# Performance work log

Hardware: AMD Instinct MI355X
Metric: run time of the kernel (lower is better)

Reference implementation:

```python
import jax, jax.numpy as jnp
import numpy as np

B=4; L=1024; NF=64; DM=256; DS=16; SCS=8; NL=4; DI=512; DTR=16; DC=4; NFM=6; NH=4; SCALES=(5,20,50)

def _ln(x,g,b):
    m=x.mean(-1,keepdims=True); v=((x-m)**2).mean(-1,keepdims=True)
    return (x-m)*jax.lax.rsqrt(v+1e-5)*g+b

def _scan(dA,dBu,C):
    # sequential selective scan: h_t = dA_t*h + dBu_t ; y_t = sum_n h_t * C_t
    def step(h,inp):
        a,bu,c=inp
        h=a*h+bu
        return h, jnp.einsum('bdn,bn->bd',h,c)
    h0=jnp.zeros(dA.shape[:1]+dA.shape[2:],dA.dtype)
    _,ys=jax.lax.scan(step,h0,(dA.swapaxes(0,1),dBu.swapaxes(0,1),C.swapaxes(0,1)))
    return ys.swapaxes(0,1)  # [B,L,DI]

def _mamba(x,g,b,inw,cw,cb,xpw,dtw,dtb,Alog,Dp,outw,ds):
    # MambaBlock: LN -> SelectiveSSM -> residual (dropout=identity in eval)
    xn=_ln(x,g,b)
    u,z=jnp.split(xn@inw.T,2,-1)
    k=cw.T[:,None,:]  # torch depthwise Conv1d weight [DI,1,DC] -> WIO [DC,1,DI]
    u=jax.lax.conv_general_dilated(u,k,(1,),[(cw.shape[1]-1,0)],dimension_numbers=('NWC','WIO','NWC'),feature_group_count=u.shape[-1])+cb
    u=jax.nn.silu(u)
    A=-jnp.exp(Alog)                     # [DI,ds]
    xd=u@xpw.T                           # [B,L,DTR+2*ds]
    dt=jax.nn.softplus(xd[...,:DTR]@dtw.T+dtb)   # [B,L,DI]
    Bm=xd[...,DTR:DTR+ds]; Cm=xd[...,DTR+ds:]
    dA=jnp.exp(dt[...,None]*A)                   # [B,L,DI,ds]
    dBu=dt[...,None]*Bm[:,:,None,:]*u[...,None]  # [B,L,DI,ds]
    y=_scan(dA,dBu,Cm)+u*Dp
    return x+(y*jax.nn.silu(z))@outw.T

def _mha(x,wqkv,bqkv,wout,bout):
    Bq,S,E=x.shape; hd=E//NH
    q,k,v=jnp.split(x@wqkv.T+bqkv,3,-1)
    sp=lambda t: t.reshape(Bq,S,NH,hd).transpose(0,2,1,3)
    att=jax.nn.softmax(jnp.einsum('bhqd,bhkd->bhqk',sp(q),sp(k))*(1.0/np.sqrt(hd)),-1)
    o=jnp.einsum('bhqk,bhkd->bhqd',att,sp(v)).transpose(0,2,1,3).reshape(Bq,S,E)
    return o@wout.T+bout

def _forward(x,in_w,in_b,in_ln_g,in_ln_b,mb_ln_g,mb_ln_b,mb_in_w,mb_conv_w,mb_conv_b,mb_xp_w,mb_dt_w,mb_dt_b,mb_Alog,mb_D,mb_out_w,sc_ln_g,sc_ln_b,sc_in_w,sc_conv_w,sc_conv_b,sc_xp_w,sc_dt_w,sc_dt_b,sc_Alog,sc_D,sc_out_w,fus_qkv_w,fus_qkv_b,fus_out_w,fus_out_b,ms_out_w,ms_out_b,sa_ln1_g,sa_ln1_b,sa_ln2_g,sa_ln2_b,sa_qkv_w,sa_qkv_b,sa_out_w,sa_out_b,sa_ff1_w,sa_ff1_b,sa_ff2_w,sa_ff2_b,ev1_w,ev1_b,ev2_w,ev2_b,ttf1_w,ttf1_b,ttf2_w,ttf2_b,emb_w,emb_b):
    gelu=lambda t: jax.nn.gelu(t,approximate=False)
    h=gelu(_ln(x@in_w.T+in_b,in_ln_g,in_ln_b))
    for i in range(NL):
        h=_mamba(h,mb_ln_g[i],mb_ln_b[i],mb_in_w[i],mb_conv_w[i],mb_conv_b[i],mb_xp_w[i],mb_dt_w[i],mb_dt_b[i],mb_Alog[i],mb_D[i],mb_out_w[i],DS)
    pooled=[]
    for i,s in enumerate(SCALES):
        p=_mamba(h[:,-s:,:],sc_ln_g[i],sc_ln_b[i],sc_in_w[i],sc_conv_w[i],sc_conv_b[i],sc_xp_w[i],sc_dt_w[i],sc_dt_b[i],sc_Alog[i],sc_D[i],sc_out_w[i],SCS)
        pooled.append(p.mean(1))  # AdaptiveAvgPool1d(1)
    stack=jnp.stack(pooled,1)  # [B,3,DM]
    fused=_mha(stack,fus_qkv_w,fus_qkv_b,fus_out_w,fus_out_b).reshape(x.shape[0],-1)@ms_out_w.T+ms_out_b
    s2=stack+_mha(_ln(stack,sa_ln1_g,sa_ln1_b),sa_qkv_w,sa_qkv_b,sa_out_w,sa_out_b)
    att=s2+(gelu(_ln(s2,sa_ln2_g,sa_ln2_b)@sa_ff1_w.T+sa_ff1_b)@sa_ff2_w.T+sa_ff2_b)
    final=fused+att.mean(1)
    ev=jax.nn.softplus(gelu(final@ev1_w.T+ev1_b)@ev2_w.T+ev2_b)
    alpha=ev+1.0
    Ssum=alpha.sum(-1,keepdims=True)
    probs=alpha/Ssum; unc=(NFM+1)/Ssum
    ttf=gelu(final@ttf1_w.T+ttf1_b)@ttf2_w.T+ttf2_b
    tm=jax.nn.softplus(ttf[:,:NFM]); ts=jnp.exp(0.5*ttf[:,NFM:])
    emb=final@emb_w.T+emb_b
    # concat of (probs, evidence, alpha, uncertainty, ttf_mean, ttf_std, embedding) -> [B,162]
    return jnp.concatenate([probs,ev,alpha,unc,tm,ts,emb],-1)

def setup_inputs():
    ks=iter(jax.random.split(jax.random.key(0),64))
    nk=lambda: next(ks)
    w=lambda *s: jax.random.normal(nk(),s,jnp.float32)*0.02
    z=lambda *s: jnp.zeros(s,jnp.float32)
    o=lambda *s: jnp.ones(s,jnp.float32)
    Al=lambda n,ds: jnp.broadcast_to(jnp.log(jnp.arange(1,ds+1,dtype=jnp.float32)),(n,DI,ds))
    return dict(x=jax.random.normal(nk(),(B,L,NF),jnp.float32),
        in_w=w(DM,NF), in_b=z(DM), in_ln_g=o(DM), in_ln_b=z(DM),
        mb_ln_g=o(NL,DM), mb_ln_b=z(NL,DM), mb_in_w=w(NL,2*DI,DM), mb_conv_w=w(NL,DI,DC), mb_conv_b=z(NL,DI),
        mb_xp_w=w(NL,DTR+2*DS,DI), mb_dt_w=w(NL,DI,DTR), mb_dt_b=z(NL,DI), mb_Alog=Al(NL,DS), mb_D=o(NL,DI), mb_out_w=w(NL,DM,DI),
        sc_ln_g=o(3,DM), sc_ln_b=z(3,DM), sc_in_w=w(3,2*DI,DM), sc_conv_w=w(3,DI,DC), sc_conv_b=z(3,DI),
        sc_xp_w=w(3,DTR+2*SCS,DI), sc_dt_w=w(3,DI,DTR), sc_dt_b=z(3,DI), sc_Alog=Al(3,SCS), sc_D=o(3,DI), sc_out_w=w(3,DM,DI),
        fus_qkv_w=w(3*DM,DM), fus_qkv_b=z(3*DM), fus_out_w=w(DM,DM), fus_out_b=z(DM), ms_out_w=w(DM,3*DM), ms_out_b=z(DM),
        sa_ln1_g=o(DM), sa_ln1_b=z(DM), sa_ln2_g=o(DM), sa_ln2_b=z(DM),
        sa_qkv_w=w(3*DM,DM), sa_qkv_b=z(3*DM), sa_out_w=w(DM,DM), sa_out_b=z(DM),
        sa_ff1_w=w(4*DM,DM), sa_ff1_b=z(4*DM), sa_ff2_w=w(DM,4*DM), sa_ff2_b=z(DM),
        ev1_w=w(DM,DM), ev1_b=z(DM), ev2_w=w(NFM+1,DM), ev2_b=z(NFM+1),
        ttf1_w=w(DM//2,DM), ttf1_b=z(DM//2), ttf2_w=w(2*NFM,DM//2), ttf2_b=z(2*NFM),
        emb_w=w(DM//2,DM), emb_b=z(DM//2))

def reference(x,in_w,in_b,in_ln_g,in_ln_b,mb_ln_g,mb_ln_b,mb_in_w,mb_conv_w,mb_conv_b,mb_xp_w,mb_dt_w,mb_dt_b,mb_Alog,mb_D,mb_out_w,sc_ln_g,sc_ln_b,sc_in_w,sc_conv_w,sc_conv_b,sc_xp_w,sc_dt_w,sc_dt_b,sc_Alog,sc_D,sc_out_w,fus_qkv_w,fus_qkv_b,fus_out_w,fus_out_b,ms_out_w,ms_out_b,sa_ln1_g,sa_ln1_b,sa_ln2_g,sa_ln2_b,sa_qkv_w,sa_qkv_b,sa_out_w,sa_out_b,sa_ff1_w,sa_ff1_b,sa_ff2_w,sa_ff2_b,ev1_w,ev1_b,ev2_w,ev2_b,ttf1_w,ttf1_b,ttf2_w,ttf2_b,emb_w,emb_b):
    return _forward(x,in_w,in_b,in_ln_g,in_ln_b,mb_ln_g,mb_ln_b,mb_in_w,mb_conv_w,mb_conv_b,mb_xp_w,mb_dt_w,mb_dt_b,mb_Alog,mb_D,mb_out_w,sc_ln_g,sc_ln_b,sc_in_w,sc_conv_w,sc_conv_b,sc_xp_w,sc_dt_w,sc_dt_b,sc_Alog,sc_D,sc_out_w,fus_qkv_w,fus_qkv_b,fus_out_w,fus_out_b,ms_out_w,ms_out_b,sa_ln1_g,sa_ln1_b,sa_ln2_g,sa_ln2_b,sa_qkv_w,sa_qkv_b,sa_out_w,sa_out_b,sa_ff1_w,sa_ff1_b,sa_ff2_w,sa_ff2_b,ev1_w,ev1_b,ev2_w,ev2_b,ttf1_w,ttf1_b,ttf2_w,ttf2_b,emb_w,emb_b)
```

## Files before the change

### kernel.cpp

```cpp
#include <hip/hip_runtime.h>
#include <math.h>


typedef short short8v __attribute__((ext_vector_type(8)));
typedef float f32x4   __attribute__((ext_vector_type(4)));

__device__ __forceinline__ float geluf(float x){ return 0.5f*x*(1.0f + erff(x*0.70710678118654752f)); }
__device__ __forceinline__ float softplusf_(float x){ return (x > 20.f) ? x : log1pf(expf(x)); }
__device__ __forceinline__ unsigned short f2bf(float f){
  unsigned int u = __float_as_uint(f);
  unsigned int r = (u + 0x7FFFu + ((u >> 16) & 1u)) >> 16;
  return (unsigned short)r;
}

__global__ __launch_bounds__(256) void k_f2b(const float* __restrict__ s,
                                             unsigned short* __restrict__ d, int n){
  int i = (blockIdx.x*256 + threadIdx.x)*4;
  if (i < n){
    float4 v = *(const float4*)(s + i);
    *(ushort4*)(d + i) = make_ushort4(f2bf(v.x), f2bf(v.y), f2bf(v.z), f2bf(v.w));
  }
}

__global__ __launch_bounds__(256) void k_inproj(
    const float* __restrict__ x, const float* __restrict__ w,
    const float* __restrict__ b, const float* __restrict__ g,
    const float* __restrict__ beta, float* __restrict__ h)
{
  __shared__ float xr[64];
  __shared__ float r1[4], r2[4];
  int row = blockIdx.x;
  int tid = threadIdx.x;
  if (tid < 64) xr[tid] = x[row*64 + tid];
  __syncthreads();
  float acc = b[tid];
  const float* wr = w + tid*64;
  #pragma unroll
  for (int k = 0; k < 64; k++) acc += xr[k]*wr[k];
  float s1 = acc, s2 = acc*acc;
  #pragma unroll
  for (int o = 32; o > 0; o >>= 1){ s1 += __shfl_down(s1,o,64); s2 += __shfl_down(s2,o,64); }
  if ((tid & 63) == 0){ r1[tid>>6] = s1; r2[tid>>6] = s2; }
  __syncthreads();
  float S1 = r1[0]+r1[1]+r1[2]+r1[3];
  float S2 = r2[0]+r2[1]+r2[2]+r2[3];
  float m = S1*(1.f/256.f);
  float var = S2*(1.f/256.f) - m*m;
  float xn = (acc - m)*rsqrtf(var + 1e-5f)*g[tid] + beta[tid];
  h[row*256 + tid] = geluf(xn);
}

__global__ __launch_bounds__(256) void k_ln(
    const float* __restrict__ src, const float* __restrict__ g, const float* __restrict__ beta,
    unsigned short* __restrict__ dst, int rows_per_b, int src_off)
{
  __shared__ float r1[4], r2[4];
  int r = blockIdx.x, tid = threadIdx.x;
  int b = r / rows_per_b, t = r % rows_per_b;
  float v = src[(b*1024 + src_off + t)*256 + tid];
  float s1 = v, s2 = v*v;
  #pragma unroll
  for (int o = 32; o > 0; o >>= 1){ s1 += __shfl_down(s1,o,64); s2 += __shfl_down(s2,o,64); }
  if ((tid & 63) == 0){ r1[tid>>6] = s1; r2[tid>>6] = s2; }
  __syncthreads();
  float S1 = r1[0]+r1[1]+r1[2]+r1[3];
  float S2 = r2[0]+r2[1]+r2[2]+r2[3];
  float m = S1*(1.f/256.f);
  float var = S2*(1.f/256.f) - m*m;
  dst[r*256 + tid] = f2bf((v - m)*rsqrtf(var + 1e-5f)*g[tid] + beta[tid]);
}

template<int MODE>
__global__ __launch_bounds__(256) void k_mm64(
    const unsigned short* __restrict__ A, const unsigned short* __restrict__ W,
    float* __restrict__ C,
    const float* __restrict__ resid, int rows_per_b, int res_off,
    float* __restrict__ pool_out, int pool_off, float pool_scale,
    int M, int N, int K)
{
  int tid = threadIdx.x;
  int wave = tid >> 6, lane = tid & 63;
  int mh = wave & 1, nh = wave >> 1;
  int m0 = blockIdx.y*64 + mh*32;
  int n0 = blockIdx.x*64 + nh*32;
  int lrow = lane & 15, kc = lane >> 4;
  f32x4 acc[2][2] = {{{0.f,0.f,0.f,0.f},{0.f,0.f,0.f,0.f}},{{0.f,0.f,0.f,0.f},{0.f,0.f,0.f,0.f}}};
  for (int k0 = 0; k0 < K; k0 += 32){
    short8v a[2], b[2];
    #pragma unroll
    for (int mi = 0; mi < 2; mi++){
      int r = m0 + mi*16 + lrow; r = min(r, M-1);
      a[mi] = *(const short8v*)(A + r*K + k0 + kc*8);
    }
    #pragma unroll
    for (int ni = 0; ni < 2; ni++){
      int c = n0 + ni*16 + lrow;
      b[ni] = *(const short8v*)(W + c*K + k0 + kc*8);
    }
    #pragma unroll
    for (int mi = 0; mi < 2; mi++)
      #pragma unroll
      for (int ni = 0; ni < 2; ni++)
        acc[mi][ni] = __builtin_amdgcn_mfma_f32_16x16x32_bf16(a[mi], b[ni], acc[mi][ni], 0, 0, 0);
  }
  int rb = kc*4;
  #pragma unroll
  for (int mi = 0; mi < 2; mi++){
    #pragma unroll
    for (int rr = 0; rr < 4; rr++){
      int grow = m0 + mi*16 + rb + rr;
      if (grow >= M) continue;
      int bb = grow / rows_per_b, t = grow % rows_per_b;
      #pragma unroll
      for (int ni = 0; ni < 2; ni++){
        int gcol = n0 + ni*16 + lrow;
        float v = acc[mi][ni][rr];
        if (MODE == 0){
          C[grow*N + gcol] = v;
        } else {
          float rv = resid[(bb*1024 + res_off + t)*256 + gcol] + v;
          if (MODE == 1) C[grow*N + gcol] = rv;
          else atomicAdd(&pool_out[bb*768 + pool_off + gcol], rv*pool_scale);
        }
      }
    }
  }
}

template<int NT>
__global__ __launch_bounds__(256) void k_mmN(
    const unsigned short* __restrict__ A, const unsigned short* __restrict__ W,
    float* __restrict__ C, int M, int K)
{
  int tid = threadIdx.x;
  int wave = tid >> 6, lane = tid & 63;
  int m0 = blockIdx.y*64 + wave*16;
  int lrow = lane & 15, kc = lane >> 4;
  f32x4 acc[NT];
  #pragma unroll
  for (int ni = 0; ni < NT; ni++) acc[ni] = (f32x4){0.f,0.f,0.f,0.f};
  for (int k0 = 0; k0 < K; k0 += 32){
    int r = m0 + lrow; r = min(r, M-1);
    short8v a = *(const short8v*)(A + r*K + k0 + kc*8);
    #pragma unroll
    for (int ni = 0; ni < NT; ni++){
      short8v b = *(const short8v*)(W + (ni*16 + lrow)*K + k0 + kc*8);
      acc[ni] = __builtin_amdgcn_mfma_f32_16x16x32_bf16(a, b, acc[ni], 0, 0, 0);
    }
  }
  int rb = kc*4;
  #pragma unroll
  for (int rr = 0; rr < 4; rr++){
    int grow = m0 + rb + rr;
    if (grow >= M) continue;
    #pragma unroll
    for (int ni = 0; ni < NT; ni++)
      C[grow*(NT*16) + ni*16 + lrow] = acc[ni][rr];
  }
}

__global__ __launch_bounds__(256) void k_conv(
    const float* __restrict__ uz, const float* __restrict__ cw, const float* __restrict__ cb,
    float* __restrict__ uc, unsigned short* __restrict__ ucb, int Lseq)
{
  int row = blockIdx.x;
  int t = row % Lseq;
  int tid = threadIdx.x;
  for (int d = tid; d < 512; d += 256){
    float acc = cb[d];
    const float* w = cw + d*4;
    #pragma unroll
    for (int k = 0; k < 4; k++){
      int ts = t - 3 + k;
      if (ts >= 0) acc += uz[(row - (3-k))*1024 + d]*w[k];
    }
    float s = acc/(1.f + expf(-acc));
    uc[row*512 + d] = s;
    ucb[row*512 + d] = f2bf(s);
  }
}

__global__ __launch_bounds__(256) void k_dt(
    const float* __restrict__ xd, const float* __restrict__ dtw, const float* __restrict__ dtb,
    float* __restrict__ dt, int xdld)
{
  __shared__ float sx[16];
  int row = blockIdx.x, tid = threadIdx.x;
  if (tid < 16) sx[tid] = xd[row*xdld + tid];
  __syncthreads();
  for (int d = tid; d < 512; d += 256){
    float acc = dtb[d];
    const float* w = dtw + d*16;
    #pragma unroll
    for (int j = 0; j < 16; j++) acc += sx[j]*w[j];
    dt[row*512 + d] = softplusf_(acc);
  }
}


template<int DS>
__global__ __launch_bounds__(64) void k_scan_p1(
    const float* __restrict__ dt, const float* __restrict__ uc,
    const float* __restrict__ xd, const float* __restrict__ Alog,
    float* __restrict__ hend, float* __restrict__ sdtb,
    int Lseq, int xdld, int NCH, int CL)
{
  const int Q = DS/4;
  __shared__ float sdt[64][64], suc[64][64];
  __shared__ float sB[64][DS];
  int tid = threadIdx.x;
  int dblk = blockIdx.x;
  int d = dblk*64 + tid;
  int b = blockIdx.y, ch = blockIdx.z;
  int t0 = ch*CL;
  float A[DS];
  #pragma unroll
  for (int n = 0; n < DS; n++) A[n] = -__expf(Alog[d*DS + n]);
  for (int e = tid; e < CL*16; e += 64){
    int t = e >> 4, q = (e & 15)*4;
    long off = (long)(b*Lseq + t0 + t)*512 + dblk*64 + q;
    *(float4*)&sdt[t][q] = *(const float4*)(dt + off);
    *(float4*)&suc[t][q] = *(const float4*)(uc + off);
  }
  for (int e = tid; e < CL*Q; e += 64){
    int t = e/Q, q = (e%Q)*4;
    *(float4*)&sB[t][q] = *(const float4*)(xd + (long)(b*Lseq + t0 + t)*xdld + 16 + q);
  }
  __syncthreads();
  float h[DS];
  #pragma unroll
  for (int n = 0; n < DS; n++) h[n] = 0.f;
  float Ssum = 0.f;
  #pragma unroll 2
  for (int t = 0; t < CL; t++){
    float dtv = sdt[t][tid];
    float uv  = suc[t][tid];
    Ssum += dtv;
    float du = dtv*uv;
    #pragma unroll
    for (int n = 0; n < DS; n++)
      h[n] = fmaf(__expf(dtv*A[n]), h[n], du*sB[t][n]);
  }
  int base = ((b*NCH + ch)*512 + d)*DS;
  #pragma unroll
  for (int q = 0; q < Q; q++)
    *(float4*)(hend + base + q*4) = make_float4(h[q*4], h[q*4+1], h[q*4+2], h[q*4+3]);
  sdtb[(b*NCH + ch)*512 + d] = Ssum;
}

__global__ __launch_bounds__(256) void k_scomb(
    const float* __restrict__ hend, const float* __restrict__ sdtb,
    const float* __restrict__ Alog, float* __restrict__ hstart, int NCH)
{
  int idx = blockIdx.x*256 + threadIdx.x;
  int low = idx & 8191;
  int n = idx & 15, d = (idx >> 4) & 511, b = idx >> 13;
  float A = -__expf(Alog[d*16 + n]);
  float hs = 0.f;
  hstart[(b*NCH)*8192 + low] = 0.f;
  for (int c = 0; c < NCH-1; c++){
    float S  = sdtb[(b*NCH + c)*512 + d];
    float he = hend[(b*NCH + c)*8192 + low];
    hs = fmaf(__expf(A*S), hs, he);
    hstart[(b*NCH + c + 1)*8192 + low] = hs;
  }
}

template<int DS>
__global__ __launch_bounds__(64) void k_scan_p3(
    const float* __restrict__ dt, const float* __restrict__ uc,
    const float* __restrict__ uz, const float* __restrict__ xd,
    const float* __restrict__ Alog, const float* __restrict__ Dp,
    const float* __restrict__ hstart, unsigned short* __restrict__ yg,
    int Lseq, int xdld, int NCH, int CL, int init0)
{
  const int Q2 = DS/2;
  __shared__ float sdt[64][64], suc[64][64], sz[64][64];
  __shared__ float sBC[64][2*DS];
  int tid = threadIdx.x;
  int dblk = blockIdx.x;
  int d = dblk*64 + tid;
  int b = blockIdx.y, ch = blockIdx.z;
  int t0 = ch*CL;
  float A[DS];
  #pragma unroll
  for (int n = 0; n < DS; n++) A[n] = -__expf(Alog[d*DS + n]);
  float Dv = Dp[d];
  for (int e = tid; e < CL*16; e += 64){
    int t = e >> 4, q = (e & 15)*4;
    long off = (long)(b*Lseq + t0 + t)*512 + dblk*64 + q;
    *(float4*)&sdt[t][q] = *(const float4*)(dt + off);
    *(float4*)&suc[t][q] = *(const float4*)(uc + off);
    *(float4*)&sz[t][q]  = *(const float4*)(uz + (long)(b*Lseq + t0 + t)*1024 + 512 + dblk*64 + q);
  }
  for (int e = tid; e < CL*Q2; e += 64){
    int t = e/Q2, q = (e%Q2)*4;
    *(float4*)&sBC[t][q] = *(const float4*)(xd + (long)(b*Lseq + t0 + t)*xdld + 16 + q);
  }
  __syncthreads();
  float h[DS];
  if (init0){
    #pragma unroll
    for (int n = 0; n < DS; n++) h[n] = 0.f;
  } else {
    int base = ((b*NCH + ch)*512 + d)*DS;
    #pragma unroll
    for (int q = 0; q < DS/4; q++){
      float4 v = *(const float4*)(hstart + base + q*4);
      h[q*4] = v.x; h[q*4+1] = v.y; h[q*4+2] = v.z; h[q*4+3] = v.w;
    }
  }
  #pragma unroll 2
  for (int t = 0; t < CL; t++){
    float dtv = sdt[t][tid];
    float uv  = suc[t][tid];
    float zv  = sz[t][tid];
    float du = dtv*uv;
    float y = 0.f;
    #pragma unroll
    for (int n = 0; n < DS; n++){
      h[n] = fmaf(__expf(dtv*A[n]), h[n], du*sBC[t][n]);
      y = fmaf(h[n], sBC[t][DS+n], y);
    }
    y = fmaf(uv, Dv, y);
    float gate = zv/(1.f + __expf(-zv));
    yg[(long)(b*Lseq + t0 + t)*512 + d] = f2bf(y*gate);
  }
}

__global__ void k_zero(float* p, int n){
  int i = blockIdx.x*256 + threadIdx.x;
  if (i < n) p[i] = 0.f;
}

template<int M, int ACT, int RES>
__global__ __launch_bounds__(256) void k_tw(
    const float* __restrict__ A, const float* __restrict__ W,
    const float* __restrict__ bias, float* __restrict__ out,
    const float* __restrict__ resid, int N, int K, int ostride, int ocoff)
{
  extern __shared__ float sx[];
  int tid = threadIdx.x;
  for (int e = tid*4; e < M*K; e += 1024)
    *(float4*)&sx[e] = *(const float4*)(A + e);
  __syncthreads();
  int wave = tid >> 6, lane = tid & 63;
  int c = blockIdx.x*4 + wave;
  if (c >= N) return;
  float acc[M];
  #pragma unroll
  for (int r = 0; r < M; r++) acc[r] = 0.f;
  for (int k = lane*4; k < K; k += 256){
    float4 w4 = *(const float4*)(W + c*K + k);
    #pragma unroll
    for (int r = 0; r < M; r++){
      float4 x4 = *(float4*)&sx[r*K + k];
      acc[r] = fmaf(x4.x,w4.x,fmaf(x4.y,w4.y,fmaf(x4.z,w4.z,fmaf(x4.w,w4.w,acc[r]))));
    }
  }
  #pragma unroll
  for (int r = 0; r < M; r++){
    #pragma unroll
    for (int o = 32; o > 0; o >>= 1) acc[r] += __shfl_down(acc[r], o, 64);
  }
  if (lane == 0){
    float bv = bias[c];
    #pragma unroll
    for (int r = 0; r < M; r++){
      float v = acc[r] + bv;
      if (ACT == 1) v = geluf(v);
      if (RES == 1) v += resid[r*256 + c];
      out[r*ostride + ocoff + c] = v;
    }
  }
}

__global__ __launch_bounds__(256) void k_t_ln(
    const float* __restrict__ src, const float* __restrict__ g, const float* __restrict__ b,
    float* __restrict__ dst)
{
  __shared__ float r1[4], r2[4];
  int r = blockIdx.x, tid = threadIdx.x;
  float v = src[r*256 + tid];
  float s1 = v, s2 = v*v;
  #pragma unroll
  for (int o = 32; o > 0; o >>= 1){ s1 += __shfl_down(s1,o,64); s2 += __shfl_down(s2,o,64); }
  if ((tid & 63) == 0){ r1[tid>>6] = s1; r2[tid>>6] = s2; }
  __syncthreads();
  float S1 = r1[0]+r1[1]+r1[2]+r1[3];
  float S2 = r2[0]+r2[1]+r2[2]+r2[3];
  float m = S1*(1.f/256.f);
  float var = S2*(1.f/256.f) - m*m;
  dst[r*256 + tid] = (v - m)*rsqrtf(var + 1e-5f)*g[tid] + b[tid];
}

__global__ __launch_bounds__(256) void k_t_att(
    const float* __restrict__ qkv, float* __restrict__ ov)
{
  __shared__ float att[36];
  int b = blockIdx.x, tid = threadIdx.x;
  if (tid < 36){
    int hh = tid/9, r = (tid%9)/3, c = tid%3;
    float s = 0.f;
    const float* qp = qkv + (b*3 + r)*768 + hh*64;
    const float* kp = qkv + (b*3 + c)*768 + 256 + hh*64;
    for (int k = 0; k < 64; k++) s += qp[k]*kp[k];
    att[hh*9 + r*3 + c] = s*0.125f;
  }
  __syncthreads();
  if (tid < 12){
    int hh = tid/3, r = tid%3;
    float a0 = att[hh*9+r*3+0], a1 = att[hh*9+r*3+1], a2 = att[hh*9+r*3+2];
    float m = fmaxf(a0, fmaxf(a1, a2));
    float e0 = expf(a0-m), e1 = expf(a1-m), e2 = expf(a2-m);
    float s = e0+e1+e2;
    att[hh*9+r*3+0] = e0/s; att[hh*9+r*3+1] = e1/s; att[hh*9+r*3+2] = e2/s;
  }
  __syncthreads();
  for (int e = tid; e < 768; e += 256){
    int p = e >> 8, i = e & 255, hh = i >> 6;
    ov[(b*3 + p)*256 + i] = att[hh*9+p*3+0]*qkv[(b*3+0)*768+512+i]
                          + att[hh*9+p*3+1]*qkv[(b*3+1)*768+512+i]
                          + att[hh*9+p*3+2]*qkv[(b*3+2)*768+512+i];
  }
}

__global__ __launch_bounds__(256) void k_t_final(
    const float* __restrict__ fusedv, const float* __restrict__ s2f, float* __restrict__ finalv)
{
  int b = blockIdx.x, c = threadIdx.x;
  finalv[b*256 + c] = fusedv[b*256 + c] +
    (s2f[(b*3+0)*256 + c] + s2f[(b*3+1)*256 + c] + s2f[(b*3+2)*256 + c])*(1.f/3.f);
}

__global__ __launch_bounds__(64) void k_t_fin(
    const float* __restrict__ evraw, const float* __restrict__ ttraw, float* __restrict__ out)
{
  __shared__ float ev[7];
  __shared__ float S;
  int b = blockIdx.x, tid = threadIdx.x;
  if (tid < 7) ev[tid] = softplusf_(evraw[b*7 + tid]);
  __syncthreads();
  if (tid == 0){
    float s = 0.f;
    for (int j = 0; j < 7; j++) s += ev[j] + 1.f;
    S = s;
  }
  __syncthreads();
  float* ob = out + b*162;
  if (tid < 7){
    float al = ev[tid] + 1.f;
    ob[tid] = al / S;
    ob[7 + tid] = ev[tid];
    ob[14 + tid] = al;
  }
  if (tid == 0) ob[21] = 7.f / S;
  if (tid < 6){
    ob[22 + tid] = softplusf_(ttraw[b*12 + tid]);
    ob[28 + tid] = expf(0.5f*ttraw[b*12 + 6 + tid]);
  }
}

extern "C" void kernel_launch(void* const* d_in, const int* in_sizes, int n_in,
                              void* d_out, int out_size, void* d_ws, size_t ws_size,
                              hipStream_t stream)
{
  const float* x         = (const float*)d_in[0];
  const float* in_w      = (const float*)d_in[1];
  const float* in_b      = (const float*)d_in[2];
  const float* in_ln_g   = (const float*)d_in[3];
  const float* in_ln_b   = (const float*)d_in[4];
  const float* mb_ln_g   = (const float*)d_in[5];
  const float* mb_ln_b   = (const float*)d_in[6];
  const float* mb_in_w   = (const float*)d_in[7];
  const float* mb_conv_w = (const float*)d_in[8];
  const float* mb_conv_b = (const float*)d_in[9];
  const float* mb_xp_w   = (const float*)d_in[10];
  const float* mb_dt_w   = (const float*)d_in[11];
  const float* mb_dt_b   = (const float*)d_in[12];
  const float* mb_Alog   = (const float*)d_in[13];
  const float* mb_D      = (const float*)d_in[14];
  const float* mb_out_w  = (const float*)d_in[15];
  const float* sc_ln_g   = (const float*)d_in[16];
  const float* sc_ln_b   = (const float*)d_in[17];
  const float* sc_in_w   = (const float*)d_in[18];
  const float* sc_conv_w = (const float*)d_in[19];
  const float* sc_conv_b = (const float*)d_in[20];
  const float* sc_xp_w   = (const float*)d_in[21];
  const float* sc_dt_w   = (const float*)d_in[22];
  const float* sc_dt_b   = (const float*)d_in[23];
  const float* sc_Alog   = (const float*)d_in[24];
  const float* sc_D      = (const float*)d_in[25];
  const float* sc_out_w  = (const float*)d_in[26];
  const float* fus_qkv_w = (const float*)d_in[27];
  const float* fus_qkv_b = (const float*)d_in[28];
  const float* fus_out_w = (const float*)d_in[29];
  const float* fus_out_b = (const float*)d_in[30];
  const float* ms_out_w  = (const float*)d_in[31];
  const float* ms_out_b  = (const float*)d_in[32];
  const float* sa_ln1_g  = (const float*)d_in[33];
  const float* sa_ln1_b  = (const float*)d_in[34];
  const float* sa_ln2_g  = (const float*)d_in[35];
  const float* sa_ln2_b  = (const float*)d_in[36];
  const float* sa_qkv_w  = (const float*)d_in[37];
  const float* sa_qkv_b  = (const float*)d_in[38];
  const float* sa_out_w  = (const float*)d_in[39];
  const float* sa_out_b  = (const float*)d_in[40];
  const float* sa_ff1_w  = (const float*)d_in[41];
  const float* sa_ff1_b  = (const float*)d_in[42];
  const float* sa_ff2_w  = (const float*)d_in[43];
  const float* sa_ff2_b  = (const float*)d_in[44];
  const float* ev1_w     = (const float*)d_in[45];
  const float* ev1_b     = (const float*)d_in[46];
  const float* ev2_w     = (const float*)d_in[47];
  const float* ev2_b     = (const float*)d_in[48];
  const float* ttf1_w    = (const float*)d_in[49];
  const float* ttf1_b    = (const float*)d_in[50];
  const float* ttf2_w    = (const float*)d_in[51];
  const float* ttf2_b    = (const float*)d_in[52];
  const float* emb_w     = (const float*)d_in[53];
  const float* emb_b     = (const float*)d_in[54];

  const int NCH = 16, CL = 64;

  float* ws = (float*)d_ws;
  float* h     = ws;
  float* uz    = h    + 1048576;
  float* uc    = uz   + 4194304;
  float* dtb_  = uc   + 2097152;
  float* xd    = dtb_ + 2097152;
  float* stack = xd   + 196608;
  float* tb    = stack + 4096;
  float* qkvF   = tb;
  float* ovF    = qkvF + 9216;
  float* moF    = ovF  + 3072;
  float* fusedv = moF  + 3072;
  float* lnbuf  = fusedv + 1024;
  float* qkvS   = lnbuf + 3072;
  float* ovS    = qkvS + 9216;
  float* s2     = ovS  + 3072;
  float* ln2r   = s2   + 3072;
  float* hid    = ln2r + 3072;
  float* s2f    = hid  + 12288;
  float* finalv = s2f  + 3072;
  float* evh    = finalv + 1024;
  float* tth    = evh  + 1024;
  float* evraw  = tth  + 512;
  float* ttraw  = evraw + 32;
  float* hend   = ttraw + 64;
  float* hstart = hend + 524288;
  float* sdtb   = hstart + 524288;
  float* fp32_end = sdtb + 32768;
  unsigned short* bfb = (unsigned short*)fp32_end;
  unsigned short* xnb    = bfb;
  unsigned short* ucb    = xnb + 1048576;
  unsigned short* ygb    = ucb + 2097152;
  unsigned short* wmbin  = ygb + 2097152;
  unsigned short* wmbout = wmbin + 1048576;
  unsigned short* wmbxp  = wmbout + 524288;
  unsigned short* wscin  = wmbxp + 98304;
  unsigned short* wscout = wscin + 786432;
  unsigned short* wscxp  = wscout + 393216;

  k_f2b<<<1024, 256, 0, stream>>>(mb_in_w,  wmbin,  1048576);
  k_f2b<<<512,  256, 0, stream>>>(mb_out_w, wmbout, 524288);
  k_f2b<<<96,   256, 0, stream>>>(mb_xp_w,  wmbxp,  98304);
  k_f2b<<<768,  256, 0, stream>>>(sc_in_w,  wscin,  786432);
  k_f2b<<<384,  256, 0, stream>>>(sc_out_w, wscout, 393216);
  k_f2b<<<48,   256, 0, stream>>>(sc_xp_w,  wscxp,  49152);

  k_inproj<<<4096, 256, 0, stream>>>(x, in_w, in_b, in_ln_g, in_ln_b, h);

  for (int l = 0; l < 4; l++){
    const float* Al = mb_Alog + l*8192;
    k_ln<<<4096, 256, 0, stream>>>(h, mb_ln_g + l*256, mb_ln_b + l*256, xnb, 1024, 0);
    {
      dim3 g(16, 64);
      k_mm64<0><<<g, 256, 0, stream>>>(xnb, wmbin + l*262144, uz,
                                       nullptr, 1, 0, nullptr, 0, 0.f, 4096, 1024, 256);
    }
    k_conv<<<4096, 256, 0, stream>>>(uz, mb_conv_w + l*2048, mb_conv_b + l*512, uc, ucb, 1024);
    {
      dim3 g(1, 64);
      k_mmN<3><<<g, 256, 0, stream>>>(ucb, wmbxp + l*24576, xd, 4096, 512);
    }
    k_dt<<<4096, 256, 0, stream>>>(xd, mb_dt_w + l*8192, mb_dt_b + l*512, dtb_, 48);
    {
      dim3 g(8, 4, NCH);
      k_scan_p1<16><<<g, 64, 0, stream>>>(dtb_, uc, xd, Al, hend, sdtb, 1024, 48, NCH, CL);
      k_scomb<<<128, 256, 0, stream>>>(hend, sdtb, Al, hstart, NCH);
      k_scan_p3<16><<<g, 64, 0, stream>>>(dtb_, uc, uz, xd, Al, mb_D + l*512,
                                          hstart, ygb, 1024, 48, NCH, CL, 0);
    }
    {
      dim3 g(4, 64);
      k_mm64<1><<<g, 256, 0, stream>>>(ygb, wmbout + l*131072, h,
                                       h, 1024, 0, nullptr, 0, 0.f, 4096, 256, 512);
    }
  }

  k_zero<<<12, 256, 0, stream>>>(stack, 3072);
  const int scales[3] = {5, 20, 50};
  for (int i = 0; i < 3; i++){
    int s = scales[i];
    int rows = 4*s;
    int mt = (rows + 63)/64;
    k_ln<<<rows, 256, 0, stream>>>(h, sc_ln_g + i*256, sc_ln_b + i*256, xnb, s, 1024 - s);
    {
      dim3 g(16, mt);
      k_mm64<0><<<g, 256, 0, stream>>>(xnb, wscin + i*262144, uz,
                                       nullptr, 1, 0, nullptr, 0, 0.f, rows, 1024, 256);
    }
    k_conv<<<rows, 256, 0, stream>>>(uz, sc_conv_w + i*2048, sc_conv_b + i*512, uc, ucb, s);
    {
      dim3 g(1, mt);
      k_mmN<2><<<g, 256, 0, stream>>>(ucb, wscxp + i*16384, xd, rows, 512);
    }
    k_dt<<<rows, 256, 0, stream>>>(xd, sc_dt_w + i*8192, sc_dt_b + i*512, dtb_, 32);
    {
      dim3 g(8, 4, 1);
      k_scan_p3<8><<<g, 64, 0, stream>>>(dtb_, uc, uz, xd, sc_Alog + i*4096, sc_D + i*512,
                                         nullptr, ygb, s, 32, 1, s, 1);
    }
    {
      dim3 g(4, mt);
      k_mm64<2><<<g, 256, 0, stream>>>(ygb, wscout + i*131072, nullptr,
                                       h, s, 1024 - s, stack, i*256, 1.f/(float)s,
                                       rows, 256, 512);
    }
  }

  float* dout = (float*)d_out;
  k_tw<12,0,0><<<192, 256, 12*256*4, stream>>>(stack, fus_qkv_w, fus_qkv_b, qkvF, nullptr, 768, 256, 768, 0);
  k_t_att<<<4, 256, 0, stream>>>(qkvF, ovF);
  k_tw<12,0,0><<<64, 256, 12*256*4, stream>>>(ovF, fus_out_w, fus_out_b, moF, nullptr, 256, 256, 256, 0);
  k_tw<4,0,0><<<64, 256, 4*768*4, stream>>>(moF, ms_out_w, ms_out_b, fusedv, nullptr, 256, 768, 256, 0);
  k_t_ln<<<12, 256, 0, stream>>>(stack, sa_ln1_g, sa_ln1_b, lnbuf);
  k_tw<12,0,0><<<192, 256, 12*256*4, stream>>>(lnbuf, sa_qkv_w, sa_qkv_b, qkvS, nullptr, 768, 256, 768, 0);
  k_t_att<<<4, 256, 0, stream>>>(qkvS, ovS);
  k_tw<12,0,1><<<64, 256, 12*256*4, stream>>>(ovS, sa_out_w, sa_out_b, s2, stack, 256, 256, 256, 0);
  k_t_ln<<<12, 256, 0, stream>>>(s2, sa_ln2_g, sa_ln2_b, ln2r);
  k_tw<12,1,0><<<256, 256, 12*256*4, stream>>>(ln2r, sa_ff1_w, sa_ff1_b, hid, nullptr, 1024, 256, 1024, 0);
  k_tw<12,0,1><<<64, 256, 12*1024*4, stream>>>(hid, sa_ff2_w, sa_ff2_b, s2f, s2, 256, 1024, 256, 0);
  k_t_final<<<4, 256, 0, stream>>>(fusedv, s2f, finalv);
  k_tw<4,1,0><<<64, 256, 4*256*4, stream>>>(finalv, ev1_w, ev1_b, evh, nullptr, 256, 256, 256, 0);
  k_tw<4,0,0><<<2, 256, 4*256*4, stream>>>(evh, ev2_w, ev2_b, evraw, nullptr, 7, 256, 7, 0);
  k_tw<4,1,0><<<32, 256, 4*256*4, stream>>>(finalv, ttf1_w, ttf1_b, tth, nullptr, 128, 256, 128, 0);
  k_tw<4,0,0><<<3, 256, 4*128*4, stream>>>(tth, ttf2_w, ttf2_b, ttraw, nullptr, 12, 128, 12, 0);
  k_tw<4,0,0><<<32, 256, 4*256*4, stream>>>(finalv, emb_w, emb_b, dout, nullptr, 128, 256, 162, 34);
  k_t_fin<<<4, 64, 0, stream>>>(evraw, ttraw, dout);
}
```

Before: 743.1 us.

## Batch weight conversion, fuse dt into xproj, restructure scan, merge scale branches and tail

All weight fp32-to-bf16 conversions now run as one launch. The dt projection and softplus are fused into the x-projection GEMM epilogue. The chunked scan's second pass is replaced by a per-row correction kernel that adds the carried-in state to locally computed outputs. The three multi-scale SSM branches run as single batched launches, and the many small tail kernels are merged into one k_tail kernel. The aim is to cut launch count and redundant recomputation, at the cost of extra yloc and Scum buffers and an exp-heavy correction step.

```diff
diff --git a/kernel.cpp b/kernel.cpp
--- a/kernel.cpp
+++ b/kernel.cpp
@@ -13,13 +13,25 @@
   return (unsigned short)r;
 }
 
-__global__ __launch_bounds__(256) void k_f2b(const float* __restrict__ s,
-                                             unsigned short* __restrict__ d, int n){
-  int i = (blockIdx.x*256 + threadIdx.x)*4;
-  if (i < n){
-    float4 v = *(const float4*)(s + i);
-    *(ushort4*)(d + i) = make_ushort4(f2bf(v.x), f2bf(v.y), f2bf(v.z), f2bf(v.w));
-  }
+__global__ __launch_bounds__(256) void k_f2b_all(
+    const float* s0, unsigned short* d0,
+    const float* s1, unsigned short* d1,
+    const float* s2, unsigned short* d2,
+    const float* s3, unsigned short* d3,
+    const float* s4, unsigned short* d4,
+    const float* s5, unsigned short* d5)
+{
+  int blk = blockIdx.x;
+  const float* s; unsigned short* d; int base;
+  if      (blk < 1024){ s=s0; d=d0; base=0; }
+  else if (blk < 1536){ s=s1; d=d1; base=1024; }
+  else if (blk < 1632){ s=s2; d=d2; base=1536; }
+  else if (blk < 2400){ s=s3; d=d3; base=1632; }
+  else if (blk < 2784){ s=s4; d=d4; base=2400; }
+  else                { s=s5; d=d5; base=2784; }
+  int i = ((blk - base)*256 + threadIdx.x)*4;
+  float4 v = *(const float4*)(s + i);
+  *(ushort4*)(d + i) = make_ushort4(f2bf(v.x), f2bf(v.y), f2bf(v.z), f2bf(v.w));
 }
 
 __global__ __launch_bounds__(256) void k_inproj(
@@ -52,12 +64,11 @@
 
 __global__ __launch_bounds__(256) void k_ln(
     const float* __restrict__ src, const float* __restrict__ g, const float* __restrict__ beta,
-    unsigned short* __restrict__ dst, int rows_per_b, int src_off)
+    unsigned short* __restrict__ dst)
 {
   __shared__ float r1[4], r2[4];
   int r = blockIdx.x, tid = threadIdx.x;
-  int b = r / rows_per_b, t = r % rows_per_b;
-  float v = src[(b*1024 + src_off + t)*256 + tid];
+  float v = src[r*256 + tid];
   float s1 = v, s2 = v*v;
   #pragma unroll
   for (int o = 32; o > 0; o >>= 1){ s1 += __shfl_down(s1,o,64); s2 += __shfl_down(s2,o,64); }
@@ -70,19 +81,52 @@
   dst[r*256 + tid] = f2bf((v - m)*rsqrtf(var + 1e-5f)*g[tid] + beta[tid]);
 }
 
-template<int MODE>
+__device__ __forceinline__ void sc_region(int r, int& z, int& roff, int& s){
+  if (r < 64){ z=0; roff=0; s=5; }
+  else if (r < 192){ z=1; roff=64; s=20; }
+  else { z=2; roff=192; s=50; }
+}
+
+__global__ __launch_bounds__(256) void k_ln_sc(
+    const float* __restrict__ h, const float* __restrict__ gb, const float* __restrict__ bb,
+    unsigned short* __restrict__ dst)
+{
+  __shared__ float r1[4], r2[4];
+  int r = blockIdx.x, tid = threadIdx.x;
+  int z, roff, s; sc_region(r, z, roff, s);
+  int local = r - roff;
+  if (local >= 4*s) return;
+  int b = local / s, t = local % s;
+  float v = h[(b*1024 + (1024 - s) + t)*256 + tid];
+  const float* g = gb + z*256; const float* be = bb + z*256;
+  float s1 = v, s2 = v*v;
+  #pragma unroll
+  for (int o = 32; o > 0; o >>= 1){ s1 += __shfl_down(s1,o,64); s2 += __shfl_down(s2,o,64); }
+  if ((tid & 63) == 0){ r1[tid>>6] = s1; r2[tid>>6] = s2; }
+  __syncthreads();
+  float S1 = r1[0]+r1[1]+r1[2]+r1[3];
+  float S2 = r2[0]+r2[1]+r2[2]+r2[3];
+  float m = S1*(1.f/256.f);
+  float var = S2*(1.f/256.f) - m*m;
+  dst[r*256 + tid] = f2bf((v - m)*rsqrtf(var + 1e-5f)*g[tid] + be[tid]);
+}
+
+template<int MODE, int SCB>
 __global__ __launch_bounds__(256) void k_mm64(
-    const unsigned short* __restrict__ A, const unsigned short* __restrict__ W,
+    const unsigned short* __restrict__ A, const unsigned short* __restrict__ Wb,
     float* __restrict__ C,
-    const float* __restrict__ resid, int rows_per_b, int res_off,
-    float* __restrict__ pool_out, int pool_off, float pool_scale,
-    int M, int N, int K)
+    const float* __restrict__ resid,
+    float* __restrict__ pool_out,
+    int M, int N, int K, int wstr)
 {
   int tid = threadIdx.x;
   int wave = tid >> 6, lane = tid & 63;
   int mh = wave & 1, nh = wave >> 1;
   int m0 = blockIdx.y*64 + mh*32;
   int n0 = blockIdx.x*64 + nh*32;
+  int z = 0, roff = 0, sc = 0;
+  const unsigned short* W = Wb;
+  if (SCB){ sc_region(blockIdx.y*64, z, roff, sc); W += z*wstr; }
   int lrow = lane & 15, kc = lane >> 4;
   f32x4 acc[2][2] = {{{0.f,0.f,0.f,0.f},{0.f,0.f,0.f,0.f}},{{0.f,0.f,0.f,0.f},{0.f,0.f,0.f,0.f}}};
   for (int k0 = 0; k0 < K; k0 += 32){
@@ -110,17 +154,21 @@
     for (int rr = 0; rr < 4; rr++){
       int grow = m0 + mi*16 + rb + rr;
       if (grow >= M) continue;
-      int bb = grow / rows_per_b, t = grow % rows_per_b;
       #pragma unroll
       for (int ni = 0; ni < 2; ni++){
         int gcol = n0 + ni*16 + lrow;
         float v = acc[mi][ni][rr];
         if (MODE == 0){
           C[grow*N + gcol] = v;
+        } else if (MODE == 1){
+          C[grow*N + gcol] = resid[grow*256 + gcol] + v;
         } else {
-          float rv = resid[(bb*1024 + res_off + t)*256 + gcol] + v;
-          if (MODE == 1) C[grow*N + gcol] = rv;
-          else atomicAdd(&pool_out[bb*768 + pool_off + gcol], rv*pool_scale);
+          int local = grow - roff;
+          if (local < 4*sc){
+            int bb2 = local / sc, t = local % sc;
+            float rv = resid[(bb2*1024 + (1024 - sc) + t)*256 + gcol] + v;
+            atomicAdd(&pool_out[bb2*768 + z*256 + gcol], rv*(1.f/(float)sc));
+          }
         }
       }
     }
@@ -128,13 +176,17 @@
 }
 
 template<int NT>
-__global__ __launch_bounds__(256) void k_mmN(
+__global__ __launch_bounds__(256) void k_mmNdt(
     const unsigned short* __restrict__ A, const unsigned short* __restrict__ W,
-    float* __restrict__ C, int M, int K)
-{
+    float* __restrict__ Cout,
+    const float* __restrict__ dtw, const float* __restrict__ dtb,
+    float* __restrict__ dtout, int M, int K)
+{
+  __shared__ float sxd[64][16];
   int tid = threadIdx.x;
   int wave = tid >> 6, lane = tid & 63;
-  int m0 = blockIdx.y*64 + wave*16;
+  int bm0 = blockIdx.y*64;
+  int m0 = bm0 + wave*16;
   int lrow = lane & 15, kc = lane >> 4;
   f32x4 acc[NT];
   #pragma unroll
@@ -152,19 +204,91 @@
   #pragma unroll
   for (int rr = 0; rr < 4; rr++){
     int grow = m0 + rb + rr;
-    if (grow >= M) continue;
     #pragma unroll
     for (int ni = 0; ni < NT; ni++)
-      C[grow*(NT*16) + ni*16 + lrow] = acc[ni][rr];
+      Cout[grow*(NT*16) + ni*16 + lrow] = acc[ni][rr];
+    sxd[wave*16 + rb + rr][lrow] = acc[0][rr];
+  }
+  __syncthreads();
+  int d0 = tid, d1 = tid + 256;
+  float w0[16], w1[16];
+  #pragma unroll
+  for (int j = 0; j < 16; j++){ w0[j] = dtw[d0*16 + j]; w1[j] = dtw[d1*16 + j]; }
+  float b0 = dtb[d0], b1 = dtb[d1];
+  for (int r = 0; r < 64; r++){
+    float a0 = b0, a1 = b1;
+    #pragma unroll
+    for (int j = 0; j < 16; j++){
+      float xv = sxd[r][j];
+      a0 = fmaf(xv, w0[j], a0);
+      a1 = fmaf(xv, w1[j], a1);
+    }
+    dtout[(bm0 + r)*512 + d0] = softplusf_(a0);
+    dtout[(bm0 + r)*512 + d1] = softplusf_(a1);
+  }
+}
+
+__global__ __launch_bounds__(256) void k_mmNdt_sc(
+    const unsigned short* __restrict__ A, const unsigned short* __restrict__ Wb,
+    float* __restrict__ Cout,
+    const float* __restrict__ dtwb, const float* __restrict__ dtbb,
+    float* __restrict__ dtout, int M, int K)
+{
+  __shared__ float sxd[64][16];
+  int tid = threadIdx.x;
+  int wave = tid >> 6, lane = tid & 63;
+  int bm0 = blockIdx.y*64;
+  int z, roff, s; sc_region(bm0, z, roff, s);
+  const unsigned short* W = Wb + z*16384;
+  const float* dtw = dtwb + z*8192;
+  const float* dtb = dtbb + z*512;
+  int m0 = bm0 + wave*16;
+  int lrow = lane & 15, kc = lane >> 4;
+  f32x4 acc[2];
+  acc[0] = (f32x4){0.f,0.f,0.f,0.f}; acc[1] = (f32x4){0.f,0.f,0.f,0.f};
+  for (int k0 = 0; k0 < K; k0 += 32){
+    int r = m0 + lrow; r = min(r, M-1);
+    short8v a = *(const short8v*)(A + r*K + k0 + kc*8);
+    #pragma unroll
+    for (int ni = 0; ni < 2; ni++){
+      short8v b = *(const short8v*)(W + (ni*16 + lrow)*K + k0 + kc*8);
+      acc[ni] = __builtin_amdgcn_mfma_f32_16x16x32_bf16(a, b, acc[ni], 0, 0, 0);
+    }
+  }
+  int rb = kc*4;
+  #pragma unroll
+  for (int rr = 0; rr < 4; rr++){
+    int grow = m0 + rb + rr;
+    #pragma unroll
+    for (int ni = 0; ni < 2; ni++)
+      Cout[grow*32 + ni*16 + lrow] = acc[ni][rr];
+    sxd[wave*16 + rb + rr][lrow] = acc[0][rr];
+  }
+  __syncthreads();
+  int d0 = tid, d1 = tid + 256;
+  float w0[16], w1[16];
+  #pragma unroll
+  for (int j = 0; j < 16; j++){ w0[j] = dtw[d0*16 + j]; w1[j] = dtw[d1*16 + j]; }
+  float b0 = dtb[d0], b1 = dtb[d1];
+  for (int r = 0; r < 64; r++){
+    float a0 = b0, a1 = b1;
+    #pragma unroll
+    for (int j = 0; j < 16; j++){
+      float xv = sxd[r][j];
+      a0 = fmaf(xv, w0[j], a0);
+      a1 = fmaf(xv, w1[j], a1);
+    }
+    dtout[(bm0 + r)*512 + d0] = softplusf_(a0);
+    dtout[(bm0 + r)*512 + d1] = softplusf_(a1);
   }
 }
 
 __global__ __launch_bounds__(256) void k_conv(
     const float* __restrict__ uz, const float* __restrict__ cw, const float* __restrict__ cb,
-    float* __restrict__ uc, unsigned short* __restrict__ ucb, int Lseq)
+    float* __restrict__ uc, unsigned short* __restrict__ ucb)
 {
   int row = blockIdx.x;
-  int t = row % Lseq;
+  int t = row & 1023;
   int tid = threadIdx.x;
   for (int d = tid; d < 512; d += 256){
     float acc = cb[d];
@@ -180,82 +304,98 @@
   }
 }
 
-__global__ __launch_bounds__(256) void k_dt(
-    const float* __restrict__ xd, const float* __restrict__ dtw, const float* __restrict__ dtb,
-    float* __restrict__ dt, int xdld)
-{
-  __shared__ float sx[16];
-  int row = blockIdx.x, tid = threadIdx.x;
-  if (tid < 16) sx[tid] = xd[row*xdld + tid];
-  __syncthreads();
+__global__ __launch_bounds__(256) void k_conv_sc(
+    const float* __restrict__ uz, const float* __restrict__ cwb, const float* __restrict__ cbb,
+    float* __restrict__ uc, unsigned short* __restrict__ ucb)
+{
+  int row = blockIdx.x;
+  int z, roff, s; sc_region(row, z, roff, s);
+  int local = row - roff;
+  if (local >= 4*s) return;
+  int t = local % s;
+  const float* cw = cwb + z*2048;
+  const float* cb = cbb + z*512;
+  int tid = threadIdx.x;
   for (int d = tid; d < 512; d += 256){
-    float acc = dtb[d];
-    const float* w = dtw + d*16;
-    #pragma unroll
-    for (int j = 0; j < 16; j++) acc += sx[j]*w[j];
-    dt[row*512 + d] = softplusf_(acc);
-  }
-}
-
-
-template<int DS>
-__global__ __launch_bounds__(64) void k_scan_p1(
+    float acc = cb[d];
+    const float* w = cw + d*4;
+    #pragma unroll
+    for (int k = 0; k < 4; k++){
+      int ts = t - 3 + k;
+      if (ts >= 0) acc += uz[(row - (3-k))*1024 + d]*w[k];
+    }
+    float sv = acc/(1.f + expf(-acc));
+    uc[row*512 + d] = sv;
+    ucb[row*512 + d] = f2bf(sv);
+  }
+}
+
+__global__ __launch_bounds__(64) void k_scan_p1y(
     const float* __restrict__ dt, const float* __restrict__ uc,
     const float* __restrict__ xd, const float* __restrict__ Alog,
     float* __restrict__ hend, float* __restrict__ sdtb,
-    int Lseq, int xdld, int NCH, int CL)
-{
-  const int Q = DS/4;
+    float* __restrict__ yloc, float* __restrict__ Scum)
+{
+  const int CL = 64, NCH = 16;
   __shared__ float sdt[64][64], suc[64][64];
-  __shared__ float sB[64][DS];
+  __shared__ float sBC[64][32];
   int tid = threadIdx.x;
   int dblk = blockIdx.x;
   int d = dblk*64 + tid;
   int b = blockIdx.y, ch = blockIdx.z;
   int t0 = ch*CL;
-  float A[DS];
-  #pragma unroll
-  for (int n = 0; n < DS; n++) A[n] = -__expf(Alog[d*DS + n]);
+  float A[16];
+  #pragma unroll
+  for (int n = 0; n < 16; n++) A[n] = -__expf(Alog[d*16 + n]);
   for (int e = tid; e < CL*16; e += 64){
     int t = e >> 4, q = (e & 15)*4;
-    long off = (long)(b*Lseq + t0 + t)*512 + dblk*64 + q;
+    long off = (long)(b*1024 + t0 + t)*512 + dblk*64 + q;
     *(float4*)&sdt[t][q] = *(const float4*)(dt + off);
     *(float4*)&suc[t][q] = *(const float4*)(uc + off);
   }
-  for (int e = tid; e < CL*Q; e += 64){
-    int t = e/Q, q = (e%Q)*4;
-    *(float4*)&sB[t][q] = *(const float4*)(xd + (long)(b*Lseq + t0 + t)*xdld + 16 + q);
-  }
-  __syncthreads();
-  float h[DS];
-  #pragma unroll
-  for (int n = 0; n < DS; n++) h[n] = 0.f;
-  float Ssum = 0.f;
+  for (int e = tid; e < CL*8; e += 64){
+    int t = e >> 3, q = (e & 7)*4;
+    *(float4*)&sBC[t][q] = *(const float4*)(xd + (long)(b*1024 + t0 + t)*48 + 16 + q);
+  }
+  __syncthreads();
+  float h[16];
+  #pragma unroll
+  for (int n = 0; n < 16; n++) h[n] = 0.f;
+  float Ss = 0.f;
   #pragma unroll 2
   for (int t = 0; t < CL; t++){
     float dtv = sdt[t][tid];
     float uv  = suc[t][tid];
-    Ssum += dtv;
+    Ss += dtv;
     float du = dtv*uv;
-    #pragma unroll
-    for (int n = 0; n < DS; n++)
-      h[n] = fmaf(__expf(dtv*A[n]), h[n], du*sB[t][n]);
-  }
-  int base = ((b*NCH + ch)*512 + d)*DS;
-  #pragma unroll
-  for (int q = 0; q < Q; q++)
+    float y = 0.f;
+    #pragma unroll
+    for (int n = 0; n < 16; n++){
+      h[n] = fmaf(__expf(dtv*A[n]), h[n], du*sBC[t][n]);
+      y = fmaf(h[n], sBC[t][16+n], y);
+    }
+    long row = (long)(b*1024 + t0 + t);
+    yloc[row*512 + d] = y;
+    Scum[row*512 + d] = Ss;
+  }
+  int base = ((b*NCH + ch)*512 + d)*16;
+  #pragma unroll
+  for (int q = 0; q < 4; q++)
     *(float4*)(hend + base + q*4) = make_float4(h[q*4], h[q*4+1], h[q*4+2], h[q*4+3]);
-  sdtb[(b*NCH + ch)*512 + d] = Ssum;
+  sdtb[(b*NCH + ch)*512 + d] = Ss;
 }
 
 __global__ __launch_bounds__(256) void k_scomb(
     const float* __restrict__ hend, const float* __restrict__ sdtb,
-    const float* __restrict__ Alog, float* __restrict__ hstart, int NCH)
-{
+    const float* __restrict__ Alog, float* __restrict__ hstart,
+    float* __restrict__ Aneg)
+{
+  const int NCH = 16;
   int idx = blockIdx.x*256 + threadIdx.x;
   int low = idx & 8191;
-  int n = idx & 15, d = (idx >> 4) & 511, b = idx >> 13;
-  float A = -__expf(Alog[d*16 + n]);
+  int d = (idx >> 4) & 511, b = idx >> 13;
+  float A = -__expf(Alog[low]);
+  if (b == 0) Aneg[low] = A;
   float hs = 0.f;
   hstart[(b*NCH)*8192 + low] = 0.f;
   for (int c = 0; c < NCH-1; c++){
@@ -266,65 +406,85 @@
   }
 }
 
-template<int DS>
-__global__ __launch_bounds__(64) void k_scan_p3(
+__global__ __launch_bounds__(256) void k_corr(
+    const float* __restrict__ yloc, const float* __restrict__ Scum,
+    const float* __restrict__ hstart, const float* __restrict__ Aneg,
+    const float* __restrict__ xd, const float* __restrict__ uc,
+    const float* __restrict__ uz, const float* __restrict__ Dp,
+    unsigned short* __restrict__ yg)
+{
+  __shared__ float sC[16];
+  int row = blockIdx.x, tid = threadIdx.x;
+  int b = row >> 10, t = row & 1023, ch = t >> 6;
+  if (tid < 16) sC[tid] = xd[row*48 + 32 + tid];
+  __syncthreads();
+  #pragma unroll
+  for (int rep = 0; rep < 2; rep++){
+    int d = tid + rep*256;
+    float Ss = Scum[row*512 + d];
+    float y  = yloc[row*512 + d];
+    const float* hs = hstart + ((b*16 + ch)*512 + d)*16;
+    const float* An = Aneg + d*16;
+    #pragma unroll
+    for (int n = 0; n < 16; n++)
+      y = fmaf(__expf(An[n]*Ss)*hs[n], sC[n], y);
+    float uv = uc[row*512 + d];
+    y = fmaf(uv, Dp[d], y);
+    float zv = uz[row*1024 + 512 + d];
+    yg[row*512 + d] = f2bf(y*(zv/(1.f + __expf(-zv))));
+  }
+}
+
+__global__ __launch_bounds__(64) void k_scan_sc(
     const float* __restrict__ dt, const float* __restrict__ uc,
     const float* __restrict__ uz, const float* __restrict__ xd,
-    const float* __restrict__ Alog, const float* __restrict__ Dp,
-    const float* __restrict__ hstart, unsigned short* __restrict__ yg,
-    int Lseq, int xdld, int NCH, int CL, int init0)
-{
-  const int Q2 = DS/2;
-  __shared__ float sdt[64][64], suc[64][64], sz[64][64];
-  __shared__ float sBC[64][2*DS];
+    const float* __restrict__ Alogb, const float* __restrict__ Dpb,
+    unsigned short* __restrict__ yg)
+{
+  __shared__ float sdt[52][64], suc[52][64], sz[52][64];
+  __shared__ float sBC[52][16];
   int tid = threadIdx.x;
   int dblk = blockIdx.x;
   int d = dblk*64 + tid;
-  int b = blockIdx.y, ch = blockIdx.z;
-  int t0 = ch*CL;
-  float A[DS];
-  #pragma unroll
-  for (int n = 0; n < DS; n++) A[n] = -__expf(Alog[d*DS + n]);
+  int b = blockIdx.y, z = blockIdx.z;
+  int s = (z==0) ? 5 : (z==1) ? 20 : 50;
+  int roff = (z==0) ? 0 : (z==1) ? 64 : 192;
+  const float* Alog = Alogb + z*4096;
+  const float* Dp   = Dpb + z*512;
+  float A[8];
+  #pragma unroll
+  for (int n = 0; n < 8; n++) A[n] = -__expf(Alog[d*8 + n]);
   float Dv = Dp[d];
-  for (int e = tid; e < CL*16; e += 64){
+  for (int e = tid; e < s*16; e += 64){
     int t = e >> 4, q = (e & 15)*4;
-    long off = (long)(b*Lseq + t0 + t)*512 + dblk*64 + q;
-    *(float4*)&sdt[t][q] = *(const float4*)(dt + off);
-    *(float4*)&suc[t][q] = *(const float4*)(uc + off);
-    *(float4*)&sz[t][q]  = *(const float4*)(uz + (long)(b*Lseq + t0 + t)*1024 + 512 + dblk*64 + q);
-  }
-  for (int e = tid; e < CL*Q2; e += 64){
-    int t = e/Q2, q = (e%Q2)*4;
-    *(float4*)&sBC[t][q] = *(const float4*)(xd + (long)(b*Lseq + t0 + t)*xdld + 16 + q);
-  }
-  __syncthreads();
-  float h[DS];
-  if (init0){
-    #pragma unroll
-    for (int n = 0; n < DS; n++) h[n] = 0.f;
-  } else {
-    int base = ((b*NCH + ch)*512 + d)*DS;
-    #pragma unroll
-    for (int q = 0; q < DS/4; q++){
-      float4 v = *(const float4*)(hstart + base + q*4);
-      h[q*4] = v.x; h[q*4+1] = v.y; h[q*4+2] = v.z; h[q*4+3] = v.w;
-    }
-  }
-  #pragma unroll 2
-  for (int t = 0; t < CL; t++){
+    long row = (long)(roff + b*s + t);
+    *(float4*)&sdt[t][q] = *(const float4*)(dt + row*512 + dblk*64 + q);
+    *(float4*)&suc[t][q] = *(const float4*)(uc + row*512 + dblk*64 + q);
+    *(float4*)&sz[t][q]  = *(const float4*)(uz + row*1024 + 512 + dblk*64 + q);
+  }
+  for (int e = tid; e < s*4; e += 64){
+    int t = e >> 2, q = (e & 3)*4;
+    long row = (long)(roff + b*s + t);
+    *(float4*)&sBC[t][q] = *(const float4*)(xd + row*32 + 16 + q);
+  }
+  __syncthreads();
+  float h[8];
+  #pragma unroll
+  for (int n = 0; n < 8; n++) h[n] = 0.f;
+  for (int t = 0; t < s; t++){
     float dtv = sdt[t][tid];
     float uv  = suc[t][tid];
     float zv  = sz[t][tid];
     float du = dtv*uv;
     float y = 0.f;
     #pragma unroll
-    for (int n = 0; n < DS; n++){
+    for (int n = 0; n < 8; n++){
       h[n] = fmaf(__expf(dtv*A[n]), h[n], du*sBC[t][n]);
-      y = fmaf(h[n], sBC[t][DS+n], y);
+      y = fmaf(h[n], sBC[t][8+n], y);
     }
     y = fmaf(uv, Dv, y);
     float gate = zv/(1.f + __expf(-zv));
-    yg[(long)(b*Lseq + t0 + t)*512 + d] = f2bf(y*gate);
+    yg[(long)(roff + b*s + t)*512 + d] = f2bf(y*gate);
   }
 }
 
@@ -333,77 +493,52 @@
   if (i < n) p[i] = 0.f;
 }
 
-template<int M, int ACT, int RES>
-__global__ __launch_bounds__(256) void k_tw(
-    const float* __restrict__ A, const float* __restrict__ W,
-    const float* __restrict__ bias, float* __restrict__ out,
-    const float* __restrict__ resid, int N, int K, int ostride, int ocoff)
-{
-  extern __shared__ float sx[];
-  int tid = threadIdx.x;
-  for (int e = tid*4; e < M*K; e += 1024)
-    *(float4*)&sx[e] = *(const float4*)(A + e);
-  __syncthreads();
+template<int M>
+__device__ __forceinline__ void wgemm(
+    const float* in, int K,
+    const float* __restrict__ W, const float* __restrict__ bias,
+    float* outp, int N, int ostr, int act,
+    const float* resid, int rstr)
+{
+  int tid = threadIdx.x;
   int wave = tid >> 6, lane = tid & 63;
-  int c = blockIdx.x*4 + wave;
-  if (c >= N) return;
-  float acc[M];
-  #pragma unroll
-  for (int r = 0; r < M; r++) acc[r] = 0.f;
-  for (int k = lane*4; k < K; k += 256){
-    float4 w4 = *(const float4*)(W + c*K + k);
+  for (int c = wave; c < N; c += 16){
+    float acc[M];
+    #pragma unroll
+    for (int r = 0; r < M; r++) acc[r] = 0.f;
+    for (int k = lane*4; k < K; k += 256){
+      float4 w4 = *(const float4*)(W + c*K + k);
+      #pragma unroll
+      for (int r = 0; r < M; r++){
+        float4 x4 = *(const float4*)(in + r*K + k);
+        acc[r] = fmaf(x4.x,w4.x,fmaf(x4.y,w4.y,fmaf(x4.z,w4.z,fmaf(x4.w,w4.w,acc[r]))));
+      }
+    }
     #pragma unroll
     for (int r = 0; r < M; r++){
-      float4 x4 = *(float4*)&sx[r*K + k];
-      acc[r] = fmaf(x4.x,w4.x,fmaf(x4.y,w4.y,fmaf(x4.z,w4.z,fmaf(x4.w,w4.w,acc[r]))));
-    }
-  }
-  #pragma unroll
-  for (int r = 0; r < M; r++){
-    #pragma unroll
-    for (int o = 32; o > 0; o >>= 1) acc[r] += __shfl_down(acc[r], o, 64);
-  }
-  if (lane == 0){
-    float bv = bias[c];
-    #pragma unroll
-    for (int r = 0; r < M; r++){
-      float v = acc[r] + bv;
-      if (ACT == 1) v = geluf(v);
-      if (RES == 1) v += resid[r*256 + c];
-      out[r*ostride + ocoff + c] = v;
-    }
-  }
-}
-
-__global__ __launch_bounds__(256) void k_t_ln(
-    const float* __restrict__ src, const float* __restrict__ g, const float* __restrict__ b,
-    float* __restrict__ dst)
-{
-  __shared__ float r1[4], r2[4];
-  int r = blockIdx.x, tid = threadIdx.x;
-  float v = src[r*256 + tid];
-  float s1 = v, s2 = v*v;
-  #pragma unroll
-  for (int o = 32; o > 0; o >>= 1){ s1 += __shfl_down(s1,o,64); s2 += __shfl_down(s2,o,64); }
-  if ((tid & 63) == 0){ r1[tid>>6] = s1; r2[tid>>6] = s2; }
-  __syncthreads();
-  float S1 = r1[0]+r1[1]+r1[2]+r1[3];
-  float S2 = r2[0]+r2[1]+r2[2]+r2[3];
-  float m = S1*(1.f/256.f);
-  float var = S2*(1.f/256.f) - m*m;
-  dst[r*256 + tid] = (v - m)*rsqrtf(var + 1e-5f)*g[tid] + b[tid];
-}
-
-__global__ __launch_bounds__(256) void k_t_att(
-    const float* __restrict__ qkv, float* __restrict__ ov)
-{
-  __shared__ float att[36];
-  int b = blockIdx.x, tid = threadIdx.x;
+      #pragma unroll
+      for (int o = 32; o > 0; o >>= 1) acc[r] += __shfl_down(acc[r], o, 64);
+    }
+    if (lane == 0){
+      float bv = bias[c];
+      #pragma unroll
+      for (int r = 0; r < M; r++){
+        float v = acc[r] + bv;
+        if (act == 1) v = geluf(v);
+        if (resid) v += resid[r*rstr + c];
+        outp[r*ostr + c] = v;
+      }
+    }
+  }
+}
+
+__device__ __forceinline__ void tail_att(const float* qkv, float* att, float* ov){
+  int tid = threadIdx.x;
   if (tid < 36){
     int hh = tid/9, r = (tid%9)/3, c = tid%3;
     float s = 0.f;
-    const float* qp = qkv + (b*3 + r)*768 + hh*64;
-    const float* kp = qkv + (b*3 + c)*768 + 256 + hh*64;
+    const float* qp = qkv + r*768 + hh*64;
+    const float* kp = qkv + c*768 + 256 + hh*64;
     for (int k = 0; k < 64; k++) s += qp[k]*kp[k];
     att[hh*9 + r*3 + c] = s*0.125f;
   }
@@ -417,47 +552,113 @@
     att[hh*9+r*3+0] = e0/s; att[hh*9+r*3+1] = e1/s; att[hh*9+r*3+2] = e2/s;
   }
   __syncthreads();
-  for (int e = tid; e < 768; e += 256){
-    int p = e >> 8, i = e & 255, hh = i >> 6;
-    ov[(b*3 + p)*256 + i] = att[hh*9+p*3+0]*qkv[(b*3+0)*768+512+i]
-                          + att[hh*9+p*3+1]*qkv[(b*3+1)*768+512+i]
-                          + att[hh*9+p*3+2]*qkv[(b*3+2)*768+512+i];
-  }
-}
-
-__global__ __launch_bounds__(256) void k_t_final(
-    const float* __restrict__ fusedv, const float* __restrict__ s2f, float* __restrict__ finalv)
-{
-  int b = blockIdx.x, c = threadIdx.x;
-  finalv[b*256 + c] = fusedv[b*256 + c] +
-    (s2f[(b*3+0)*256 + c] + s2f[(b*3+1)*256 + c] + s2f[(b*3+2)*256 + c])*(1.f/3.f);
-}
-
-__global__ __launch_bounds__(64) void k_t_fin(
-    const float* __restrict__ evraw, const float* __restrict__ ttraw, float* __restrict__ out)
-{
-  __shared__ float ev[7];
-  __shared__ float S;
+  if (tid < 768){
+    int p = tid >> 8, i = tid & 255, hh = i >> 6;
+    ov[p*256 + i] = att[hh*9+p*3+0]*qkv[0*768+512+i]
+                  + att[hh*9+p*3+1]*qkv[1*768+512+i]
+                  + att[hh*9+p*3+2]*qkv[2*768+512+i];
+  }
+  __syncthreads();
+}
+
+__device__ __forceinline__ void tail_ln3(const float* in, float* outp,
+    const float* g, const float* bb, float* red1, float* red2){
+  int tid = threadIdx.x;
+  float v = 0.f;
+  int p = tid >> 8, c = tid & 255;
+  if (tid < 768){
+    v = in[p*256 + c];
+    float s1 = v, s2 = v*v;
+    #pragma unroll
+    for (int o = 32; o > 0; o >>= 1){ s1 += __shfl_down(s1,o,64); s2 += __shfl_down(s2,o,64); }
+    if ((tid & 63) == 0){ red1[tid>>6] = s1; red2[tid>>6] = s2; }
+  }
+  __syncthreads();
+  if (tid < 768){
+    float S1 = red1[p*4+0]+red1[p*4+1]+red1[p*4+2]+red1[p*4+3];
+    float S2 = red2[p*4+0]+red2[p*4+1]+red2[p*4+2]+red2[p*4+3];
+    float m = S1*(1.f/256.f);
+    float var = S2*(1.f/256.f) - m*m;
+    outp[p*256 + c] = (v - m)*rsqrtf(var + 1e-5f)*g[c] + bb[c];
+  }
+  __syncthreads();
+}
+
+__global__ __launch_bounds__(1024) void k_tail(
+    const float* __restrict__ stack,
+    const float* fqw, const float* fqb, const float* fow, const float* fob,
+    const float* msw, const float* msb,
+    const float* l1g, const float* l1b, const float* l2g, const float* l2b,
+    const float* sqw, const float* sqb, const float* sow, const float* sob,
+    const float* f1w, const float* f1b, const float* f2w, const float* f2b,
+    const float* e1w, const float* e1b, const float* e2w, const float* e2b,
+    const float* t1w, const float* t1b, const float* t2w, const float* t2b,
+    const float* ew, const float* eb,
+    float* __restrict__ out)
+{
+  __shared__ float st[768], lnr[768], qkv[2304], att[36], ov[768], mo[768];
+  __shared__ float s2[768], hid[3072], s2f[768], fusedv[256], finalv[256];
+  __shared__ float evh[256], tth[128], sv[48];
+  __shared__ float red1[12], red2[12];
   int b = blockIdx.x, tid = threadIdx.x;
-  if (tid < 7) ev[tid] = softplusf_(evraw[b*7 + tid]);
+
+  if (tid < 768) st[tid] = stack[b*768 + tid];
+  __syncthreads();
+
+  wgemm<3>(st, 256, fqw, fqb, qkv, 768, 768, 0, nullptr, 0);
+  __syncthreads();
+  tail_att(qkv, att, ov);
+  wgemm<3>(ov, 256, fow, fob, mo, 256, 256, 0, nullptr, 0);
+  __syncthreads();
+  wgemm<1>(mo, 768, msw, msb, fusedv, 256, 256, 0, nullptr, 0);
+  __syncthreads();
+
+  tail_ln3(st, lnr, l1g, l1b, red1, red2);
+  wgemm<3>(lnr, 256, sqw, sqb, qkv, 768, 768, 0, nullptr, 0);
+  __syncthreads();
+  tail_att(qkv, att, ov);
+  wgemm<3>(ov, 256, sow, sob, s2, 256, 256, 0, st, 256);
+  __syncthreads();
+  tail_ln3(s2, lnr, l2g, l2b, red1, red2);
+  wgemm<3>(lnr, 256, f1w, f1b, hid, 1024, 1024, 1, nullptr, 0);
+  __syncthreads();
+  wgemm<3>(hid, 1024, f2w, f2b, s2f, 256, 256, 0, s2, 256);
+  __syncthreads();
+
+  if (tid < 256)
+    finalv[tid] = fusedv[tid] + (s2f[tid] + s2f[256+tid] + s2f[512+tid])*(1.f/3.f);
+  __syncthreads();
+
+  wgemm<1>(finalv, 256, e1w, e1b, evh, 256, 256, 1, nullptr, 0);
+  __syncthreads();
+  wgemm<1>(evh, 256, e2w, e2b, sv, 7, 7, 0, nullptr, 0);
+  __syncthreads();
+  wgemm<1>(finalv, 256, t1w, t1b, tth, 128, 128, 1, nullptr, 0);
+  __syncthreads();
+  wgemm<1>(tth, 128, t2w, t2b, sv + 16, 12, 12, 0, nullptr, 0);
+  float* ob = out + b*162;
+  wgemm<1>(finalv, 256, ew, eb, ob + 34, 128, 128, 0, nullptr, 0);
+  __syncthreads();
+
+  if (tid < 7) sv[32 + tid] = softplusf_(sv[tid]);
   __syncthreads();
   if (tid == 0){
     float s = 0.f;
-    for (int j = 0; j < 7; j++) s += ev[j] + 1.f;
-    S = s;
-  }
-  __syncthreads();
-  float* ob = out + b*162;
+    for (int j = 0; j < 7; j++) s += sv[32+j] + 1.f;
+    sv[40] = s;
+  }
+  __syncthreads();
+  float S = sv[40];
   if (tid < 7){
-    float al = ev[tid] + 1.f;
+    float ev = sv[32 + tid], al = ev + 1.f;
     ob[tid] = al / S;
-    ob[7 + tid] = ev[tid];
+    ob[7 + tid] = ev;
     ob[14 + tid] = al;
   }
   if (tid == 0) ob[21] = 7.f / S;
   if (tid < 6){
-    ob[22 + tid] = softplusf_(ttraw[b*12 + tid]);
-    ob[28 + tid] = expf(0.5f*ttraw[b*12 + 6 + tid]);
+    ob[22 + tid] = softplusf_(sv[16 + tid]);
+    ob[28 + tid] = expf(0.5f*sv[16 + 6 + tid]);
   }
 }
 
@@ -521,8 +722,6 @@
   const float* emb_w     = (const float*)d_in[53];
   const float* emb_b     = (const float*)d_in[54];
 
-  const int NCH = 16, CL = 64;
-
   float* ws = (float*)d_ws;
   float* h     = ws;
   float* uz    = h    + 1048576;
@@ -530,27 +729,13 @@
   float* dtb_  = uc   + 2097152;
   float* xd    = dtb_ + 2097152;
   float* stack = xd   + 196608;
-  float* tb    = stack + 4096;
-  float* qkvF   = tb;
-  float* ovF    = qkvF + 9216;
-  float* moF    = ovF  + 3072;
-  float* fusedv = moF  + 3072;
-  float* lnbuf  = fusedv + 1024;
-  float* qkvS   = lnbuf + 3072;
-  float* ovS    = qkvS + 9216;
-  float* s2     = ovS  + 3072;
-  float* ln2r   = s2   + 3072;
-  float* hid    = ln2r + 3072;
-  float* s2f    = hid  + 12288;
-  float* finalv = s2f  + 3072;
-  float* evh    = finalv + 1024;
-  float* tth    = evh  + 1024;
-  float* evraw  = tth  + 512;
-  float* ttraw  = evraw + 32;
-  float* hend   = ttraw + 64;
+  float* hend   = stack + 4096;
   float* hstart = hend + 524288;
   float* sdtb   = hstart + 524288;
-  float* fp32_end = sdtb + 32768;
+  float* yloc   = sdtb + 32768;
+  float* Scum   = yloc + 2097152;
+  float* Aneg   = Scum + 2097152;
+  float* fp32_end = Aneg + 8192;
   unsigned short* bfb = (unsigned short*)fp32_end;
   unsigned short* xnb    = bfb;
   unsigned short* ucb    = xnb + 1048576;
@@ -562,91 +747,69 @@
   unsigned short* wscout = wscin + 786432;
   unsigned short* wscxp  = wscout + 393216;
 
-  k_f2b<<<1024, 256, 0, stream>>>(mb_in_w,  wmbin,  1048576);
-  k_f2b<<<512,  256, 0, stream>>>(mb_out_w, wmbout, 524288);
-  k_f2b<<<96,   256, 0, stream>>>(mb_xp_w,  wmbxp,  98304);
-  k_f2b<<<768,  256, 0, stream>>>(sc_in_w,  wscin,  786432);
-  k_f2b<<<384,  256, 0, stream>>>(sc_out_w, wscout, 393216);
-  k_f2b<<<48,   256, 0, stream>>>(sc_xp_w,  wscxp,  49152);
+  k_f2b_all<<<2832, 256, 0, stream>>>(mb_in_w, wmbin, mb_out_w, wmbout, mb_xp_w, wmbxp,
+                                      sc_in_w, wscin, sc_out_w, wscout, sc_xp_w, wscxp);
 
   k_inproj<<<4096, 256, 0, stream>>>(x, in_w, in_b, in_ln_g, in_ln_b, h);
 
   for (int l = 0; l < 4; l++){
     const float* Al = mb_Alog + l*8192;
-    k_ln<<<4096, 256, 0, stream>>>(h, mb_ln_g + l*256, mb_ln_b + l*256, xnb, 1024, 0);
+    k_ln<<<4096, 256, 0, stream>>>(h, mb_ln_g + l*256, mb_ln_b + l*256, xnb);
     {
       dim3 g(16, 64);
-      k_mm64<0><<<g, 256, 0, stream>>>(xnb, wmbin + l*262144, uz,
-                                       nullptr, 1, 0, nullptr, 0, 0.f, 4096, 1024, 256);
-    }
-    k_conv<<<4096, 256, 0, stream>>>(uz, mb_conv_w + l*2048, mb_conv_b + l*512, uc, ucb, 1024);
+      k_mm64<0,0><<<g, 256, 0, stream>>>(xnb, wmbin + l*262144, uz,
+                                         nullptr, nullptr, 4096, 1024, 256, 0);
+    }
+    k_conv<<<4096, 256, 0, stream>>>(uz, mb_conv_w + l*2048, mb_conv_b + l*512, uc, ucb);
     {
       dim3 g(1, 64);
-      k_mmN<3><<<g, 256, 0, stream>>>(ucb, wmbxp + l*24576, xd, 4096, 512);
-    }
-    k_dt<<<4096, 256, 0, stream>>>(xd, mb_dt_w + l*8192, mb_dt_b + l*512, dtb_, 48);
+      k_mmNdt<3><<<g, 256, 0, stream>>>(ucb, wmbxp + l*24576, xd,
+                                        mb_dt_w + l*8192, mb_dt_b + l*512, dtb_, 4096, 512);
+    }
     {
-      dim3 g(8, 4, NCH);
-      k_scan_p1<16><<<g, 64, 0, stream>>>(dtb_, uc, xd, Al, hend, sdtb, 1024, 48, NCH, CL);
-      k_scomb<<<128, 256, 0, stream>>>(hend, sdtb, Al, hstart, NCH);
-      k_scan_p3<16><<<g, 64, 0, stream>>>(dtb_, uc, uz, xd, Al, mb_D + l*512,
-                                          hstart, ygb, 1024, 48, NCH, CL, 0);
+      dim3 g(8, 4, 16);
+      k_scan_p1y<<<g, 64, 0, stream>>>(dtb_, uc, xd, Al, hend, sdtb, yloc, Scum);
+      k_scomb<<<128, 256, 0, stream>>>(hend, sdtb, Al, hstart, Aneg);
+      k_corr<<<4096, 256, 0, stream>>>(yloc, Scum, hstart, Aneg, xd, uc, uz,
+                                       mb_D + l*512, ygb);
     }
     {
       dim3 g(4, 64);
-      k_mm64<1><<<g, 256, 0, stream>>>(ygb, wmbout + l*131072, h,
-                                       h, 1024, 0, nullptr, 0, 0.f, 4096, 256, 512);
+      k_mm64<1,0><<<g, 256, 0, stream>>>(ygb, wmbout + l*131072, h,
+                                         h, nullptr, 4096, 256, 512, 0);
     }
   }
 
   k_zero<<<12, 256, 0, stream>>>(stack, 3072);
-  const int scales[3] = {5, 20, 50};
-  for (int i = 0; i < 3; i++){
-    int s = scales[i];
-    int rows = 4*s;
-    int mt = (rows + 63)/64;
-    k_ln<<<rows, 256, 0, stream>>>(h, sc_ln_g + i*256, sc_ln_b + i*256, xnb, s, 1024 - s);
-    {
-      dim3 g(16, mt);
-      k_mm64<0><<<g, 256, 0, stream>>>(xnb, wscin + i*262144, uz,
-                                       nullptr, 1, 0, nullptr, 0, 0.f, rows, 1024, 256);
-    }
-    k_conv<<<rows, 256, 0, stream>>>(uz, sc_conv_w + i*2048, sc_conv_b + i*512, uc, ucb, s);
-    {
-      dim3 g(1, mt);
-      k_mmN<2><<<g, 256, 0, stream>>>(ucb, wscxp + i*16384, xd, rows, 512);
-    }
-    k_dt<<<rows, 256, 0, stream>>>(xd, sc_dt_w + i*8192, sc_dt_b + i*512, dtb_, 32);
-    {
-      dim3 g(8, 4, 1);
-      k_scan_p3<8><<<g, 64, 0, stream>>>(dtb_, uc, uz, xd, sc_Alog + i*4096, sc_D + i*512,
-                                         nullptr, ygb, s, 32, 1, s, 1);
-    }
-    {
-      dim3 g(4, mt);
-      k_mm64<2><<<g, 256, 0, stream>>>(ygb, wscout + i*131072, nullptr,
-                                       h, s, 1024 - s, stack, i*256, 1.f/(float)s,
-                                       rows, 256, 512);
-    }
-  }
-
-  float* dout = (float*)d_out;
-  k_tw<12,0,0><<<192, 256, 12*256*4, stream>>>(stack, fus_qkv_w, fus_qkv_b, qkvF, nullptr, 768, 256, 768, 0);
-  k_t_att<<<4, 256, 0, stream>>>(qkvF, ovF);
-  k_tw<12,0,0><<<64, 256, 12*256*4, stream>>>(ovF, fus_out_w, fus_out_b, moF, nullptr, 256, 256, 256, 0);
-  k_tw<4,0,0><<<64, 256, 4*768*4, stream>>>(moF, ms_out_w, ms_out_b, fusedv, nullptr, 256, 768, 256, 0);
-  k_t_ln<<<12, 256, 0, stream>>>(stack, sa_ln1_g, sa_ln1_b, lnbuf);
-  k_tw<12,0,0><<<192, 256, 12*256*4, stream>>>(lnbuf, sa_qkv_w, sa_qkv_b, qkvS, nullptr, 768, 256, 768, 0);
-  k_t_att<<<4, 256, 0, stream>>>(qkvS, ovS);
-  k_tw<12,0,1><<<64, 256, 12*256*4, stream>>>(ovS, sa_out_w, sa_out_b, s2, stack, 256, 256, 256, 0);
-  k_t_ln<<<12, 256, 0, stream>>>(s2, sa_ln2_g, sa_ln2_b, ln2r);
-  k_tw<12,1,0><<<256, 256, 12*256*4, stream>>>(ln2r, sa_ff1_w, sa_ff1_b, hid, nullptr, 1024, 256, 1024, 0);
-  k_tw<12,0,1><<<64, 256, 12*1024*4, stream>>>(hid, sa_ff2_w, sa_ff2_b, s2f, s2, 256, 1024, 256, 0);
-  k_t_final<<<4, 256, 0, stream>>>(fusedv, s2f, finalv);
-  k_tw<4,1,0><<<64, 256, 4*256*4, stream>>>(finalv, ev1_w, ev1_b, evh, nullptr, 256, 256, 256, 0);
-  k_tw<4,0,0><<<2, 256, 4*256*4, stream>>>(evh, ev2_w, ev2_b, evraw, nullptr, 7, 256, 7, 0);
-  k_tw<4,1,0><<<32, 256, 4*256*4, stream>>>(finalv, ttf1_w, ttf1_b, tth, nullptr, 128, 256, 128, 0);
-  k_tw<4,0,0><<<3, 256, 4*128*4, stream>>>(tth, ttf2_w, ttf2_b, ttraw, nullptr, 12, 128, 12, 0);
-  k_tw<4,0,0><<<32, 256, 4*256*4, stream>>>(finalv, emb_w, emb_b, dout, nullptr, 128, 256, 162, 34);
-  k_t_fin<<<4, 64, 0, stream>>>(evraw, ttraw, dout);
-}
+  k_ln_sc<<<448, 256, 0, stream>>>(h, sc_ln_g, sc_ln_b, xnb);
+  {
+    dim3 g(16, 7);
+    k_mm64<0,1><<<g, 256, 0, stream>>>(xnb, wscin, uz, nullptr, nullptr,
+                                       448, 1024, 256, 262144);
+  }
+  k_conv_sc<<<448, 256, 0, stream>>>(uz, sc_conv_w, sc_conv_b, uc, ucb);
+  {
+    dim3 g(1, 7);
+    k_mmNdt_sc<<<g, 256, 0, stream>>>(ucb, wscxp, xd, sc_dt_w, sc_dt_b, dtb_, 448, 512);
+  }
+  {
+    dim3 g(8, 4, 3);
+    k_scan_sc<<<g, 64, 0, stream>>>(dtb_, uc, uz, xd, sc_Alog, sc_D, ygb);
+  }
+  {
+    dim3 g(4, 7);
+    k_mm64<2,1><<<g, 256, 0, stream>>>(ygb, wscout, nullptr, h, stack,
+                                       448, 256, 512, 131072);
+  }
+
+  k_tail<<<4, 1024, 0, stream>>>(stack,
+      fus_qkv_w, fus_qkv_b, fus_out_w, fus_out_b,
+      ms_out_w, ms_out_b,
+      sa_ln1_g, sa_ln1_b, sa_ln2_g, sa_ln2_b,
+      sa_qkv_w, sa_qkv_b, sa_out_w, sa_out_b,
+      sa_ff1_w, sa_ff1_b, sa_ff2_w, sa_ff2_b,
+      ev1_w, ev1_b, ev2_w, ev2_b,
+      ttf1_w, ttf1_b, ttf2_w, ttf2_b,
+      emb_w, emb_b,
+      (float*)d_out);
+}
```

Result: slower. 1.048 ms (+41.0%).
